# Optimization experiments

Hardware: AMD Instinct MI355X
Metric: run time of the kernel (lower is better)

Reference implementation:

```python
import jax, jax.numpy as jnp
import numpy as np

C = 256
NUM_HEADS = 8
GROUPS = 32
EPS = 1e-5


def setup_inputs() -> dict:
    key = jax.random.key(0)
    ks = jax.random.split(key, 7)
    B, D, H, W = 1, 16, 16, 16
    x = jax.random.normal(ks[0], (B, C, D, H, W), dtype=jnp.float32)
    # GroupNorm affine params (torch default: weight=1, bias=0; randomize slightly)
    gn_gamma = 1.0 + 0.02 * jax.random.normal(ks[1], (C,), dtype=jnp.float32)
    gn_beta = 0.02 * jax.random.normal(ks[2], (C,), dtype=jnp.float32)
    # 1x1x1 Conv3d == pointwise linear over channels
    qkv_w = jax.random.normal(ks[3], (3 * C, C), dtype=jnp.float32) / np.sqrt(C)
    qkv_b = 0.01 * jax.random.normal(ks[4], (3 * C,), dtype=jnp.float32)
    proj_w = jax.random.normal(ks[5], (C, C), dtype=jnp.float32) / np.sqrt(C)
    proj_b = 0.01 * jax.random.normal(ks[6], (C,), dtype=jnp.float32)
    return {"x": x, "gn_gamma": gn_gamma, "gn_beta": gn_beta,
            "qkv_w": qkv_w, "qkv_b": qkv_b, "proj_w": proj_w, "proj_b": proj_b}


def _group_norm(x, gamma, beta):
    B, Cc, D, H, W = x.shape
    xg = x.reshape(B, GROUPS, -1)  # [B, G, (C/G)*D*H*W]
    mean = xg.mean(axis=2, keepdims=True)
    var = xg.var(axis=2, keepdims=True)
    xn = ((xg - mean) * jax.lax.rsqrt(var + EPS)).reshape(B, Cc, D, H, W)
    return xn * gamma[None, :, None, None, None] + beta[None, :, None, None, None]


def reference(x, gn_gamma, gn_beta, qkv_w, qkv_b, proj_w, proj_b):
    B, Cc, D, H, W = x.shape
    N = D * H * W
    heads = NUM_HEADS
    hd = Cc // heads
    scale = hd ** -0.5

    xn = _group_norm(x, gn_gamma, gn_beta)
    # 1x1x1 conv -> pointwise linear over channel dim
    h = jnp.einsum('bcn,oc->bon', xn.reshape(B, Cc, N), qkv_w) + qkv_b[None, :, None]
    # match torch: reshape(B,3,heads,hd,N).permute(1,0,2,4,3)
    qkv = h.reshape(B, 3, heads, hd, N).transpose(1, 0, 2, 4, 3)  # [3,B,heads,N,hd]
    q, k, v = qkv[0], qkv[1], qkv[2]
    attn = jax.nn.softmax(jnp.einsum('bhnd,bhmd->bhnm', q, k) * scale, axis=-1)
    out = jnp.einsum('bhnm,bhmd->bhnd', attn, v)  # [B,heads,N,hd]
    # match torch: transpose(1,2).reshape(B,C,D,H,W)
    out = out.transpose(0, 2, 1, 3).reshape(B, Cc, D, H, W)
    out = jnp.einsum('bcn,oc->bon', out.reshape(B, Cc, N), proj_w) + proj_b[None, :, None]
    return x + out.reshape(B, Cc, D, H, W)
```

## Files before the change

kernel.cpp:

```cpp
#include <hip/hip_runtime.h>
#include <hip/hip_bf16.h>
#include <cstddef>
#include <cstdint>

#define NTOK 4096
#define CCH  256
#define HEADS 8
#define HD    32
#define QSCALE 0.25503494f

typedef __attribute__((ext_vector_type(8)))  short short8;
typedef __attribute__((ext_vector_type(4)))  short short4v;
typedef __attribute__((ext_vector_type(16))) float f32x16;

__device__ __forceinline__ unsigned short f2bf(float x) {
    unsigned u = __builtin_bit_cast(unsigned, x);
    u = (u + 0x7fffu + ((u >> 16) & 1u)) >> 16;
    return (unsigned short)u;
}
__device__ __forceinline__ unsigned packbf2(float a, float b) {
    unsigned r;
    asm("v_cvt_pk_bf16_f32 %0, %1, %2" : "=v"(r) : "v"(a), "v"(b));
    return r;
}
__device__ __forceinline__ float exp2hw(float x) {
    float r;
    asm("v_exp_f32 %0, %1" : "=v"(r) : "v"(x));
    return r;
}

#define GLDS(gsrc, ldst) \
  __builtin_amdgcn_global_load_lds((const __attribute__((address_space(1))) unsigned int*)(const void*)(gsrc), \
                                   (__attribute__((address_space(3))) unsigned int*)(void*)(ldst), 16, 0, 0)

#define CROW(r, hi) (((r) & 3) + 8 * ((r) >> 2) + 4 * (hi))

__global__ __launch_bounds__(256) void gn_part_kernel(
    const float* __restrict__ X, float2* __restrict__ part)
{
    int c = blockIdx.x, tid = threadIdx.x;
    const float4* xr = (const float4*)(X + (size_t)c * NTOK);
    float s = 0.f, ss = 0.f;
    #pragma unroll
    for (int i = 0; i < 4; i++) {
        float4 v = xr[tid + i * 256];
        s  += (v.x + v.y) + (v.z + v.w);
        ss += (v.x*v.x + v.y*v.y) + (v.z*v.z + v.w*v.w);
    }
    #pragma unroll
    for (int off = 32; off >= 1; off >>= 1) {
        s  += __shfl_down(s, off, 64);
        ss += __shfl_down(ss, off, 64);
    }
    __shared__ float rs[4], rss[4];
    int wid = tid >> 6, lane = tid & 63;
    if (lane == 0) { rs[wid] = s; rss[wid] = ss; }
    __syncthreads();
    if (tid == 0) {
        part[c] = make_float2(rs[0] + rs[1] + rs[2] + rs[3],
                              rss[0] + rss[1] + rss[2] + rss[3]);
    }
}

__global__ __launch_bounds__(256) void prep_kernel(
    const float* __restrict__ X, const float2* __restrict__ part,
    const float* __restrict__ gamma, const float* __restrict__ beta,
    const float* __restrict__ qkvw, const float* __restrict__ projw,
    unsigned short* __restrict__ Xt, unsigned short* __restrict__ Wqb,
    unsigned short* __restrict__ Wpb)
{
    int bi = blockIdx.x, tid = threadIdx.x;
    if (bi >= 256) {
        const float* src; unsigned short* dst;
        if (bi < 268) { src = qkvw + (size_t)(bi - 256) * 16384; dst = Wqb + (size_t)(bi - 256) * 16384; }
        else          { src = projw + (size_t)(bi - 268) * 16384; dst = Wpb + (size_t)(bi - 268) * 16384; }
        #pragma unroll
        for (int i = 0; i < 16; i++) {
            float4 v = *(const float4*)(src + (size_t)tid * 4 + (size_t)i * 1024);
            short4v w;
            w[0] = (short)f2bf(v.x); w[1] = (short)f2bf(v.y);
            w[2] = (short)f2bf(v.z); w[3] = (short)f2bf(v.w);
            *(short4v*)(dst + (size_t)tid * 4 + (size_t)i * 1024) = w;
        }
        return;
    }
    __shared__ float plds[64 * 65];
    __shared__ float gmean[8], grstd[8];
    int ci = bi >> 6, ni = bi & 63;
    if (tid < 8) {
        int g = ci * 8 + tid;
        float s = 0.f, ss = 0.f;
        #pragma unroll
        for (int k = 0; k < 8; k++) {
            float2 p = part[g * 8 + k];
            s += p.x; ss += p.y;
        }
        float mean = s * (1.f / 32768.f);
        float var  = ss * (1.f / 32768.f) - mean * mean;
        gmean[tid] = mean;
        grstd[tid] = rsqrtf(var + 1e-5f);
    }
    __syncthreads();
    #pragma unroll
    for (int i = 0; i < 4; i++) {
        int cl = (tid >> 4) + i * 16;
        int c  = ci * 64 + cl;
        int gl = cl >> 3;
        float scv = gamma[c] * grstd[gl];
        float tcv = beta[c] - gmean[gl] * scv;
        float4 v = *(const float4*)(X + (size_t)c * NTOK + ni * 64 + (tid & 15) * 4);
        float* row = plds + cl * 65 + (tid & 15) * 4;
        row[0] = v.x * scv + tcv; row[1] = v.y * scv + tcv;
        row[2] = v.z * scv + tcv; row[3] = v.w * scv + tcv;
    }
    __syncthreads();
    int nw = tid >> 2, c4 = (tid & 3) * 16;
    unsigned short tmp[16];
    #pragma unroll
    for (int i = 0; i < 16; i++) tmp[i] = f2bf(plds[(c4 + i) * 65 + nw]);
    unsigned short* dst = Xt + (size_t)(ni * 64 + nw) * CCH + ci * 64 + c4;
    *(short8*)dst       = *(short8*)&tmp[0];
    *(short8*)(dst + 8) = *(short8*)&tmp[8];
}

__global__ __launch_bounds__(256) void qkv_mfma_kernel(
    const unsigned short* __restrict__ Wqb, const unsigned short* __restrict__ Xt,
    const float* __restrict__ qkvb,
    unsigned short* __restrict__ Qb, unsigned short* __restrict__ Kbf,
    unsigned short* __restrict__ Vtb)
{
    __shared__ __align__(16) char vlds[16384];
    const int tid = threadIdx.x;
    const int wid = tid >> 6, lane = tid & 63;
    const int l31 = lane & 31, hi = lane >> 5;
    const int bo = blockIdx.x >> 5, ng = blockIdx.x & 31;
    const int o0 = bo * 32;
    const int n0 = ng * 128 + wid * 32;

    const unsigned short* ap = Xt + (size_t)(n0 + l31) * CCH + hi * 8;
    const unsigned short* bp = Wqb + (size_t)(o0 + l31) * CCH + hi * 8;

    f32x16 acc;
    #pragma unroll
    for (int i = 0; i < 16; i++) acc[i] = 0.f;
    #pragma unroll 4
    for (int ks = 0; ks < 16; ks++) {
        short8 af = *(const short8*)(ap + ks * 16);
        short8 bf = *(const short8*)(bp + ks * 16);
        acc = __builtin_amdgcn_mfma_f32_32x32x16_bf16(af, bf, acc, 0, 0, 0);
    }

    const int t3 = bo >> 3;
    const int h  = (o0 >> 5) & 7;
    const float bias = qkvb[o0 + l31];

    if (t3 != 2) {
        unsigned short* dst = ((t3 == 0) ? Qb : Kbf) + (size_t)h * NTOK * HD + l31;
        const float scl = (t3 == 0) ? QSCALE : 1.0f;
        #pragma unroll
        for (int r = 0; r < 16; r++) {
            int n = n0 + CROW(r, hi);
            dst[(size_t)n * HD] = f2bf((acc[r] + bias) * scl);
        }
    } else {
        char* my = vlds + wid * 4096;
        #pragma unroll
        for (int r = 0; r < 16; r++) {
            int row = CROW(r, hi);
            *(float*)(my + row * 128 + ((l31 * 4) ^ ((row & 7) << 4))) = acc[r] + bias;
        }
        unsigned short tmp[16];
        #pragma unroll
        for (int i = 0; i < 16; i++) {
            int n = hi * 16 + i;
            tmp[i] = f2bf(*(const float*)(my + n * 128 + ((l31 * 4) ^ ((n & 7) << 4))));
        }
        unsigned short* vd = Vtb + ((size_t)h * HD + l31) * NTOK + n0 + hi * 16;
        *(short8*)vd       = *(short8*)&tmp[0];
        *(short8*)(vd + 8) = *(short8*)&tmp[8];
    }
}

__global__ __launch_bounds__(256, 4) void attn_mfma_kernel(
    const unsigned short* __restrict__ Qb, const unsigned short* __restrict__ Kbf,
    const unsigned short* __restrict__ Vtb, unsigned short* __restrict__ att_t)
{
    __shared__ __align__(16) char ldsbuf[32768];
    __shared__ float lsum[4][32];
    const int tid = threadIdx.x;
    const int wid = tid >> 6, lane = tid & 63;
    const int l31 = lane & 31, hi = lane >> 5;
    const int bid = blockIdx.x;
    const int h    = bid & 7;
    const int base = (bid >> 3) & 15;
    const int j0   = (bid >> 7) * 32;

    const char* Khb = (const char*)(Kbf + (size_t)h * NTOK * HD) + (size_t)wid * 65536;
    const char* Vhb = (const char*)(Vtb + (size_t)h * HD * NTOK) + (size_t)wid * 2048;

    auto swz = [](int b) { return b ^ ((b >> 2) & 3); };

    int koff[2], voff[2];
    #pragma unroll
    for (int x = 0; x < 2; x++) {
        int so = swz(l31 * 4 + x * 2 + hi) * 16;
        koff[x] = so;
        voff[x] = 2048 + so;
    }

    const int pk0 = swz(lane), pk1 = swz(lane + 64);
    const char* srcK0 = Khb + pk0 * 16;
    const char* srcK1 = Khb + pk1 * 16;
    const char* srcV0 = Vhb + (size_t)(pk0 >> 2) * 8192 + (pk0 & 3) * 16;
    const char* srcV1 = Vhb + (size_t)(pk1 >> 2) * 8192 + (pk1 & 3) * 16;
    char* myLDS = ldsbuf + wid * 8192;

#define STAGE(tt, bb) do { \
    char* _db = myLDS + (bb) * 4096; \
    GLDS(srcK0 + (size_t)(tt) * 2048, _db); \
    GLDS(srcK1 + (size_t)(tt) * 2048, _db + 1024); \
    GLDS(srcV0 + (size_t)(tt) * 64,   _db + 2048); \
    GLDS(srcV1 + (size_t)(tt) * 64,   _db + 3072); \
} while (0)

    const unsigned short* qp = Qb + ((size_t)h * NTOK + base + 16 * (size_t)(j0 + l31)) * HD + hi * 8;
    short8 qf0 = *(const short8*)qp;
    short8 qf1 = *(const short8*)(qp + 16);

    f32x16 oacc;
    #pragma unroll
    for (int i = 0; i < 16; i++) oacc[i] = 0.f;
    const f32x16 zero = oacc;
    float l = 0.f;

    STAGE(0, 0);

    #pragma unroll 1
    for (int t = 0; t < 32; t++) {
        if (t < 31) {
            STAGE(t + 1, (t + 1) & 1);
            asm volatile("s_waitcnt vmcnt(4)" ::: "memory");
        } else {
            asm volatile("s_waitcnt vmcnt(0)" ::: "memory");
        }
        const char* kb = myLDS + (t & 1) * 4096;
        short8 kf0 = *(const short8*)(kb + koff[0]);
        short8 kf1 = *(const short8*)(kb + koff[1]);
        f32x16 s = __builtin_amdgcn_mfma_f32_32x32x16_bf16(kf0, qf0, zero, 0, 0, 0);
        s = __builtin_amdgcn_mfma_f32_32x32x16_bf16(kf1, qf1, s, 0, 0, 0);

        float p[16];
        #pragma unroll
        for (int r = 0; r < 16; r++) p[r] = exp2hw(s[r]);
        l += (((p[0]+p[1]) + (p[2]+p[3])) + ((p[4]+p[5]) + (p[6]+p[7])))
           + (((p[8]+p[9]) + (p[10]+p[11])) + ((p[12]+p[13]) + (p[14]+p[15])));

        short8 vf0 = *(const short8*)(kb + voff[0]);
        short8 vf1 = *(const short8*)(kb + voff[1]);

        #pragma unroll
        for (int m = 0; m < 2; m++) {
            const int b8 = m * 8;
            unsigned A0 = packbf2(p[b8 + 0], p[b8 + 1]);
            unsigned A1 = packbf2(p[b8 + 2], p[b8 + 3]);
            unsigned B0 = packbf2(p[b8 + 4], p[b8 + 5]);
            unsigned B1 = packbf2(p[b8 + 6], p[b8 + 7]);
            asm volatile("v_permlane32_swap_b32 %0, %1" : "+v"(A0), "+v"(B0));
            asm volatile("v_permlane32_swap_b32 %0, %1" : "+v"(A1), "+v"(B1));
            union { unsigned u[4]; short8 v; } pa;
            pa.u[0] = A0; pa.u[1] = A1; pa.u[2] = B0; pa.u[3] = B1;
            oacc = __builtin_amdgcn_mfma_f32_32x32x16_bf16(
                pa.v, (m == 0) ? vf0 : vf1, oacc, 0, 0, 0);
        }
    }
#undef STAGE

    l += __shfl_xor(l, 32, 64);
    #pragma unroll
    for (int r = 0; r < 16; r++) {
        int row = CROW(r, hi);
        *(float*)(myLDS + row * 128 + ((l31 * 4) ^ ((row & 7) << 4))) = oacc[r];
    }
    if (lane < 32) lsum[wid][lane] = l;
    __syncthreads();

    const int d = tid >> 3, j4 = (tid & 7) * 4;
    unsigned short ob[4];
    #pragma unroll
    for (int jj = 0; jj < 4; jj++) {
        int row = j4 + jj;
        float lt = (lsum[0][row] + lsum[1][row]) + (lsum[2][row] + lsum[3][row]);
        int so = row * 128 + ((d * 4) ^ ((row & 7) << 4));
        float a = (*(const float*)(ldsbuf + so)          + *(const float*)(ldsbuf + 8192 + so))
                + (*(const float*)(ldsbuf + 16384 + so)  + *(const float*)(ldsbuf + 24576 + so));
        ob[jj] = f2bf(a / lt);
    }
    unsigned short* dst = att_t + ((size_t)(base * 256 + h * 32 + d)) * CCH + j0 + j4;
    *(short4v*)dst = *(short4v*)ob;
}

__global__ __launch_bounds__(256) void proj_mfma_kernel(
    const unsigned short* __restrict__ Wpb, const unsigned short* __restrict__ att_t,
    const float* __restrict__ X, const float* __restrict__ pb,
    float* __restrict__ out)
{
    const int tid = threadIdx.x;
    const int wid = tid >> 6, lane = tid & 63;
    const int l31 = lane & 31, hi = lane >> 5;
    const int ot = blockIdx.x >> 5, pg = blockIdx.x & 31;
    const int o0 = ot * 32;
    const int p0 = pg * 128 + wid * 32;

    const unsigned short* ap = Wpb + (size_t)(o0 + l31) * CCH + hi * 8;
    const unsigned short* bp = att_t + (size_t)(p0 + l31) * CCH + hi * 8;

    f32x16 acc;
    #pragma unroll
    for (int i = 0; i < 16; i++) acc[i] = 0.f;
    #pragma unroll 4
    for (int ks = 0; ks < 16; ks++) {
        short8 af = *(const short8*)(ap + ks * 16);
        short8 bf = *(const short8*)(bp + ks * 16);
        acc = __builtin_amdgcn_mfma_f32_32x32x16_bf16(af, bf, acc, 0, 0, 0);
    }
    #pragma unroll
    for (int r = 0; r < 16; r++) {
        int o = o0 + CROW(r, hi);
        size_t ofs = (size_t)o * NTOK + p0 + l31;
        out[ofs] = X[ofs] + pb[o] + acc[r];
    }
}

extern "C" void kernel_launch(void* const* d_in, const int* in_sizes, int n_in,
                              void* d_out, int out_size, void* d_ws, size_t ws_size,
                              hipStream_t stream)
{
    const float* x     = (const float*)d_in[0];
    const float* gamma = (const float*)d_in[1];
    const float* beta  = (const float*)d_in[2];
    const float* qkvw  = (const float*)d_in[3];
    const float* qkvb  = (const float*)d_in[4];
    const float* projw = (const float*)d_in[5];
    const float* projb = (const float*)d_in[6];
    float* out = (float*)d_out;

    char* ws = (char*)d_ws;
    const size_t MB = 1024 * 1024;
    float2* part = (float2*)ws;
    unsigned short* Xt    = (unsigned short*)(ws + 4096);
    unsigned short* Wqb   = (unsigned short*)(ws + 4096 + 2*MB);
    unsigned short* Wpb   = Wqb + 768 * 256;
    unsigned short* Qb    = Wpb + 256 * 256;
    unsigned short* Kbf   = Qb + HEADS * NTOK * HD;
    unsigned short* Vtb   = Kbf + HEADS * NTOK * HD;
    unsigned short* att_t = Vtb + HEADS * NTOK * HD;

    gn_part_kernel<<<256, 256, 0, stream>>>(x, part);
    prep_kernel<<<272, 256, 0, stream>>>(x, part, gamma, beta, qkvw, projw, Xt, Wqb, Wpb);
    qkv_mfma_kernel<<<768, 256, 0, stream>>>(Wqb, Xt, qkvb, Qb, Kbf, Vtb);
    attn_mfma_kernel<<<1024, 256, 0, stream>>>(Qb, Kbf, Vtb, att_t);
    proj_mfma_kernel<<<256, 256, 0, stream>>>(Wpb, att_t, x, projb, out);
}
```

Baseline: 68.95 us.

## Process two query tiles per attention block with four-stage K/V pipeline

Each attention block now handles 64 query rows (two 32-row MFMA tiles) instead of 32, so every K/V tile staged in LDS is reused across both query tiles, halving K/V global traffic and the grid size. The LDS ring grows from two to four buffers with a prefetch distance of three tiles, and the XOR swizzle is dropped in favour of plain layouts plus a padded 148-byte stride for the final reduction. The costs are doubled LDS use (64KB) and more registers, with occupancy lowered to 2 blocks per SIMD set. The unswizzled K/V LDS reads may also cause bank conflicts.

Result: faster. 66.55 us (-3.5%).

```diff
diff --git a/kernel.cpp b/kernel.cpp
--- a/kernel.cpp
+++ b/kernel.cpp
@@ -181,39 +181,29 @@
     }
 }
 
-__global__ __launch_bounds__(256, 4) void attn_mfma_kernel(
+__global__ __launch_bounds__(256, 2) void attn_mfma_kernel(
     const unsigned short* __restrict__ Qb, const unsigned short* __restrict__ Kbf,
     const unsigned short* __restrict__ Vtb, unsigned short* __restrict__ att_t)
 {
-    __shared__ __align__(16) char ldsbuf[32768];
-    __shared__ float lsum[4][32];
+    __shared__ __align__(16) char ldsbuf[65536];
+    __shared__ float lsum[4][64];
     const int tid = threadIdx.x;
     const int wid = tid >> 6, lane = tid & 63;
     const int l31 = lane & 31, hi = lane >> 5;
     const int bid = blockIdx.x;
     const int h    = bid & 7;
-    const int base = (bid >> 3) & 15;
-    const int j0   = (bid >> 7) * 32;
+    const int g    = bid >> 3;
+    const int base = g & 15;
+    const int j0   = (g >> 4) * 64;
 
     const char* Khb = (const char*)(Kbf + (size_t)h * NTOK * HD) + (size_t)wid * 65536;
     const char* Vhb = (const char*)(Vtb + (size_t)h * HD * NTOK) + (size_t)wid * 2048;
 
-    auto swz = [](int b) { return b ^ ((b >> 2) & 3); };
-
-    int koff[2], voff[2];
-    #pragma unroll
-    for (int x = 0; x < 2; x++) {
-        int so = swz(l31 * 4 + x * 2 + hi) * 16;
-        koff[x] = so;
-        voff[x] = 2048 + so;
-    }
-
-    const int pk0 = swz(lane), pk1 = swz(lane + 64);
-    const char* srcK0 = Khb + pk0 * 16;
-    const char* srcK1 = Khb + pk1 * 16;
-    const char* srcV0 = Vhb + (size_t)(pk0 >> 2) * 8192 + (pk0 & 3) * 16;
-    const char* srcV1 = Vhb + (size_t)(pk1 >> 2) * 8192 + (pk1 & 3) * 16;
-    char* myLDS = ldsbuf + wid * 8192;
+    const char* srcK0 = Khb + l31 * 64 + hi * 16;
+    const char* srcK1 = Khb + l31 * 64 + 32 + hi * 16;
+    const char* srcV0 = Vhb + (size_t)l31 * 8192 + hi * 16;
+    const char* srcV1 = Vhb + (size_t)l31 * 8192 + 32 + hi * 16;
+    char* myLDS = ldsbuf + wid * 16384;
 
 #define STAGE(tt, bb) do { \
     char* _db = myLDS + (bb) * 4096; \
@@ -223,80 +213,112 @@
     GLDS(srcV1 + (size_t)(tt) * 64,   _db + 3072); \
 } while (0)
 
-    const unsigned short* qp = Qb + ((size_t)h * NTOK + base + 16 * (size_t)(j0 + l31)) * HD + hi * 8;
-    short8 qf0 = *(const short8*)qp;
-    short8 qf1 = *(const short8*)(qp + 16);
-
-    f32x16 oacc;
-    #pragma unroll
-    for (int i = 0; i < 16; i++) oacc[i] = 0.f;
-    const f32x16 zero = oacc;
-    float l = 0.f;
+    const int koff0 = l31 * 16 + hi * 512;
+    const int koff1 = l31 * 16 + 1024 + hi * 512;
+    const int voff0 = 2048 + koff0;
+    const int voff1 = 2048 + koff1;
+
+    const unsigned short* qpA = Qb + ((size_t)h * NTOK + base + 16 * (size_t)(j0 + l31)) * HD + hi * 8;
+    const unsigned short* qpB = qpA + (size_t)32 * 16 * HD;
+    short8 qfA0 = *(const short8*)qpA;
+    short8 qfA1 = *(const short8*)(qpA + 16);
+    short8 qfB0 = *(const short8*)qpB;
+    short8 qfB1 = *(const short8*)(qpB + 16);
+
+    f32x16 oaccA, oaccB;
+    #pragma unroll
+    for (int i = 0; i < 16; i++) { oaccA[i] = 0.f; oaccB[i] = 0.f; }
+    const f32x16 zero = oaccA;
+    float lA = 0.f, lB = 0.f;
 
     STAGE(0, 0);
+    STAGE(1, 1);
+    STAGE(2, 2);
 
     #pragma unroll 1
     for (int t = 0; t < 32; t++) {
-        if (t < 31) {
-            STAGE(t + 1, (t + 1) & 1);
-            asm volatile("s_waitcnt vmcnt(4)" ::: "memory");
-        } else {
-            asm volatile("s_waitcnt vmcnt(0)" ::: "memory");
-        }
-        const char* kb = myLDS + (t & 1) * 4096;
-        short8 kf0 = *(const short8*)(kb + koff[0]);
-        short8 kf1 = *(const short8*)(kb + koff[1]);
-        f32x16 s = __builtin_amdgcn_mfma_f32_32x32x16_bf16(kf0, qf0, zero, 0, 0, 0);
-        s = __builtin_amdgcn_mfma_f32_32x32x16_bf16(kf1, qf1, s, 0, 0, 0);
-
-        float p[16];
-        #pragma unroll
-        for (int r = 0; r < 16; r++) p[r] = exp2hw(s[r]);
-        l += (((p[0]+p[1]) + (p[2]+p[3])) + ((p[4]+p[5]) + (p[6]+p[7])))
-           + (((p[8]+p[9]) + (p[10]+p[11])) + ((p[12]+p[13]) + (p[14]+p[15])));
-
-        short8 vf0 = *(const short8*)(kb + voff[0]);
-        short8 vf1 = *(const short8*)(kb + voff[1]);
+        asm volatile("s_waitcnt vmcnt(8)" ::: "memory");
+        const int ts = (t + 3 < 32) ? (t + 3) : 31;
+        STAGE(ts, (t + 3) & 3);
+
+        const char* kb = myLDS + (t & 3) * 4096;
+        short8 kf0 = *(const short8*)(kb + koff0);
+        short8 kf1 = *(const short8*)(kb + koff1);
+
+        f32x16 sA = __builtin_amdgcn_mfma_f32_32x32x16_bf16(kf0, qfA0, zero, 0, 0, 0);
+        f32x16 sB = __builtin_amdgcn_mfma_f32_32x32x16_bf16(kf0, qfB0, zero, 0, 0, 0);
+        sA = __builtin_amdgcn_mfma_f32_32x32x16_bf16(kf1, qfA1, sA, 0, 0, 0);
+        sB = __builtin_amdgcn_mfma_f32_32x32x16_bf16(kf1, qfB1, sB, 0, 0, 0);
+
+        short8 vf0 = *(const short8*)(kb + voff0);
+        short8 vf1 = *(const short8*)(kb + voff1);
+
+        float pA[16], pB[16];
+        #pragma unroll
+        for (int r = 0; r < 16; r++) pA[r] = exp2hw(sA[r]);
+        #pragma unroll
+        for (int r = 0; r < 16; r++) pB[r] = exp2hw(sB[r]);
+        lA += (((pA[0]+pA[1]) + (pA[2]+pA[3])) + ((pA[4]+pA[5]) + (pA[6]+pA[7])))
+            + (((pA[8]+pA[9]) + (pA[10]+pA[11])) + ((pA[12]+pA[13]) + (pA[14]+pA[15])));
+        lB += (((pB[0]+pB[1]) + (pB[2]+pB[3])) + ((pB[4]+pB[5]) + (pB[6]+pB[7])))
+            + (((pB[8]+pB[9]) + (pB[10]+pB[11])) + ((pB[12]+pB[13]) + (pB[14]+pB[15])));
 
         #pragma unroll
         for (int m = 0; m < 2; m++) {
             const int b8 = m * 8;
-            unsigned A0 = packbf2(p[b8 + 0], p[b8 + 1]);
-            unsigned A1 = packbf2(p[b8 + 2], p[b8 + 3]);
-            unsigned B0 = packbf2(p[b8 + 4], p[b8 + 5]);
-            unsigned B1 = packbf2(p[b8 + 6], p[b8 + 7]);
+            unsigned A0 = packbf2(pA[b8 + 0], pA[b8 + 1]);
+            unsigned A1 = packbf2(pA[b8 + 2], pA[b8 + 3]);
+            unsigned B0 = packbf2(pA[b8 + 4], pA[b8 + 5]);
+            unsigned B1 = packbf2(pA[b8 + 6], pA[b8 + 7]);
             asm volatile("v_permlane32_swap_b32 %0, %1" : "+v"(A0), "+v"(B0));
             asm volatile("v_permlane32_swap_b32 %0, %1" : "+v"(A1), "+v"(B1));
             union { unsigned u[4]; short8 v; } pa;
             pa.u[0] = A0; pa.u[1] = A1; pa.u[2] = B0; pa.u[3] = B1;
-            oacc = __builtin_amdgcn_mfma_f32_32x32x16_bf16(
-                pa.v, (m == 0) ? vf0 : vf1, oacc, 0, 0, 0);
+            oaccA = __builtin_amdgcn_mfma_f32_32x32x16_bf16(
+                pa.v, (m == 0) ? vf0 : vf1, oaccA, 0, 0, 0);
+        }
+        #pragma unroll
+        for (int m = 0; m < 2; m++) {
+            const int b8 = m * 8;
+            unsigned A0 = packbf2(pB[b8 + 0], pB[b8 + 1]);
+            unsigned A1 = packbf2(pB[b8 + 2], pB[b8 + 3]);
+            unsigned B0 = packbf2(pB[b8 + 4], pB[b8 + 5]);
+            unsigned B1 = packbf2(pB[b8 + 6], pB[b8 + 7]);
+            asm volatile("v_permlane32_swap_b32 %0, %1" : "+v"(A0), "+v"(B0));
+            asm volatile("v_permlane32_swap_b32 %0, %1" : "+v"(A1), "+v"(B1));
+            union { unsigned u[4]; short8 v; } pa;
+            pa.u[0] = A0; pa.u[1] = A1; pa.u[2] = B0; pa.u[3] = B1;
+            oaccB = __builtin_amdgcn_mfma_f32_32x32x16_bf16(
+                pa.v, (m == 0) ? vf0 : vf1, oaccB, 0, 0, 0);
         }
     }
 #undef STAGE
 
-    l += __shfl_xor(l, 32, 64);
+    lA += __shfl_xor(lA, 32, 64);
+    lB += __shfl_xor(lB, 32, 64);
+    char* st = myLDS;
     #pragma unroll
     for (int r = 0; r < 16; r++) {
-        int row = CROW(r, hi);
-        *(float*)(myLDS + row * 128 + ((l31 * 4) ^ ((row & 7) << 4))) = oacc[r];
-    }
-    if (lane < 32) lsum[wid][lane] = l;
+        int rowA = CROW(r, hi);
+        *(float*)(st + rowA * 148 + l31 * 4) = oaccA[r];
+        *(float*)(st + (rowA + 32) * 148 + l31 * 4) = oaccB[r];
+    }
+    if (lane < 32) { lsum[wid][l31] = lA; lsum[wid][32 + l31] = lB; }
     __syncthreads();
 
-    const int d = tid >> 3, j4 = (tid & 7) * 4;
-    unsigned short ob[4];
-    #pragma unroll
-    for (int jj = 0; jj < 4; jj++) {
-        int row = j4 + jj;
-        float lt = (lsum[0][row] + lsum[1][row]) + (lsum[2][row] + lsum[3][row]);
-        int so = row * 128 + ((d * 4) ^ ((row & 7) << 4));
-        float a = (*(const float*)(ldsbuf + so)          + *(const float*)(ldsbuf + 8192 + so))
-                + (*(const float*)(ldsbuf + 16384 + so)  + *(const float*)(ldsbuf + 24576 + so));
-        ob[jj] = f2bf(a / lt);
-    }
-    unsigned short* dst = att_t + ((size_t)(base * 256 + h * 32 + d)) * CCH + j0 + j4;
-    *(short4v*)dst = *(short4v*)ob;
+    const int d = tid >> 3, q8 = (tid & 7) * 8;
+    unsigned short ob[8];
+    #pragma unroll
+    for (int i = 0; i < 8; i++) {
+        int q = q8 + i;
+        float lt = (lsum[0][q] + lsum[1][q]) + (lsum[2][q] + lsum[3][q]);
+        int so = q * 148 + d * 4;
+        float a = (*(const float*)(ldsbuf + so)          + *(const float*)(ldsbuf + 16384 + so))
+                + (*(const float*)(ldsbuf + 32768 + so)  + *(const float*)(ldsbuf + 49152 + so));
+        ob[i] = f2bf(a / lt);
+    }
+    unsigned short* dst = att_t + (size_t)(base * 256 + h * 32 + d) * CCH + j0 + q8;
+    *(short8*)dst = *(short8*)ob;
 }
 
 __global__ __launch_bounds__(256) void proj_mfma_kernel(
@@ -358,6 +380,6 @@
     gn_part_kernel<<<256, 256, 0, stream>>>(x, part);
     prep_kernel<<<272, 256, 0, stream>>>(x, part, gamma, beta, qkvw, projw, Xt, Wqb, Wpb);
     qkv_mfma_kernel<<<768, 256, 0, stream>>>(Wqb, Xt, qkvb, Qb, Kbf, Vtb);
-    attn_mfma_kernel<<<1024, 256, 0, stream>>>(Qb, Kbf, Vtb, att_t);
+    attn_mfma_kernel<<<512, 256, 0, stream>>>(Qb, Kbf, Vtb, att_t);
     proj_mfma_kernel<<<256, 256, 0, stream>>>(Wpb, att_t, x, projb, out);
 }
```
